# Optimization experiments

Hardware: AMD Instinct MI355X
Metric: run time of the kernel (lower is better)

The kernel has to match this reference:

```python
import jax, jax.numpy as jnp
import numpy as np

B, N, H = 32, 2048, 128
L4H = 4 * H  # concatenated (c0,h0,c1,h1) embedding dim


def _lstm_cell(x, c, h, Wx, Wh, b):
    g = x @ Wx + h @ Wh + b                      # [B,N,4H]
    i, f, gg, o = jnp.split(g, 4, axis=-1)
    c_new = jax.nn.sigmoid(f) * c + jax.nn.sigmoid(i) * jnp.tanh(gg)
    h_new = jax.nn.sigmoid(o) * jnp.tanh(c_new)
    return c_new, h_new


def setup_inputs() -> dict:
    key = jax.random.key(0)
    ks = jax.random.split(key, 20)
    s = 0.05
    inp = {
        'node_embeddings': jax.random.normal(ks[0], (B, N, H), jnp.float32),
        'c0': jax.random.normal(ks[1], (B, N, H), jnp.float32),
        'h0': jax.random.normal(ks[2], (B, N, H), jnp.float32),
        'c1': jax.random.normal(ks[3], (B, N, H), jnp.float32),
        'h1': jax.random.normal(ks[4], (B, N, H), jnp.float32),
        'instruction_pointer': jax.random.uniform(ks[5], (B, N), jnp.float32),
        'Wx0': s * jax.random.normal(ks[6], (H, 4 * H), jnp.float32),
        'Wh0': s * jax.random.normal(ks[7], (H, 4 * H), jnp.float32),
        'b0': jnp.zeros((4 * H,), jnp.float32),
        'Wx1': s * jax.random.normal(ks[8], (H, 4 * H), jnp.float32),
        'Wh1': s * jax.random.normal(ks[9], (H, 4 * H), jnp.float32),
        'b1': jnp.zeros((4 * H,), jnp.float32),
        'raise_W': s * jax.random.normal(ks[10], (L4H, 2), jnp.float32),
        'raise_b': jnp.zeros((2,), jnp.float32),
        'branch_W': s * jax.random.normal(ks[11], (L4H, 2), jnp.float32),
        'branch_b': jnp.zeros((2,), jnp.float32),
        'true_indexes': jax.random.randint(ks[12], (B, N), 0, N, jnp.int32),
        'false_indexes': jax.random.randint(ks[13], (B, N), 0, N, jnp.int32),
        'raise_indexes': jax.random.randint(ks[14], (B, N), 0, N, jnp.int32),
        'exit_node_indexes': jax.random.randint(ks[15], (B,), 0, N, jnp.int32),
        'raise_node_indexes': jax.random.randint(ks[16], (B,), 0, N, jnp.int32),
        'current_step': jnp.zeros((B,), jnp.int32),
        'step_limits': jax.random.randint(ks[17], (B,), 1, 100, jnp.int32),
    }
    return inp


def reference(node_embeddings, c0, h0, c1, h1, instruction_pointer,
              Wx0, Wh0, b0, Wx1, Wh1, b1, raise_W, raise_b, branch_W, branch_b,
              true_indexes, false_indexes, raise_indexes,
              exit_node_indexes, raise_node_indexes, current_step, step_limits):
    num_nodes = node_embeddings.shape[1]

    # --- execute: stacked 2-layer LSTM per node (vectorized over B,N) ---
    c0n, h0n = _lstm_cell(node_embeddings, c0, h0, Wx0, Wh0, b0)
    c1n, h1n = _lstm_cell(h0n, c1, h1, Wx1, Wh1, b1)
    old = (c0, h0, c1, h1)
    contrib = (c0n, h0n, c1n, h1n)

    # --- mask exit and raise nodes: keep old hidden state there ---
    node_ids = jnp.arange(num_nodes)[None, :]                  # [1,N]
    m_exit = node_ids == exit_node_indexes[:, None]            # [B,N]
    m_raise = node_ids == raise_node_indexes[:, None]          # [B,N]
    m_keep = (m_exit | m_raise)[..., None]                     # raise_in_ipagnn=True
    contrib = tuple(jnp.where(m_keep, o, c) for o, c in zip(old, contrib))

    # --- raise / branch decisions ---
    emb = jnp.concatenate(contrib, axis=-1)                    # [B,N,4H]
    raise_dec = jax.nn.softmax(emb @ raise_W + raise_b, axis=-1)
    raise_dec = jnp.where(m_exit[..., None], jnp.array([0.0, 1.0], raise_dec.dtype), raise_dec)
    branch_dec = jax.nn.softmax(emb @ branch_W + branch_b, axis=-1)

    p_raise = raise_dec[..., 0]
    p_noraise = raise_dec[..., 1]
    p_true = p_noraise * branch_dec[..., 0]
    p_false = p_noraise * branch_dec[..., 1]

    seg = jax.vmap(lambda d, i: jax.ops.segment_sum(d, i, num_segments=num_nodes))

    # --- instruction pointer update (scatter-add over soft edges) ---
    ip = instruction_pointer
    ip_new = (seg(p_raise * ip, raise_indexes)
              + seg(p_true * ip, true_indexes)
              + seg(p_false * ip, false_indexes))               # [B,N]

    # --- hidden-state aggregation, weighted by instruction pointer ---
    denom = (ip_new + 1e-7)[..., None]                          # [B,N,1]
    wr = (p_raise * ip)[..., None]
    wt = (p_true * ip)[..., None]
    wf = (p_false * ip)[..., None]
    agg = tuple((seg(hc * wr, raise_indexes)
                 + seg(hc * wt, true_indexes)
                 + seg(hc * wf, false_indexes)) / denom
                for hc in contrib)

    # --- keep old state if example already hit its step limit ---
    live = (current_step < step_limits)                         # [B]
    ip_fin = jnp.where(live[:, None], ip_new, ip)
    hid_fin = tuple(jnp.where(live[:, None, None], a, o) for a, o in zip(agg, old))

    # pack carry: (c0,h0,c1,h1) embedding + instruction pointer -> [B,N,4H+1]
    return jnp.concatenate(list(hid_fin) + [ip_fin[..., None]], axis=-1)
```

## Files before the change

### kernel.cpp

```cpp
#include <hip/hip_runtime.h>
#include <hip/hip_bf16.h>

constexpr int Bc  = 32;
constexpr int Nc  = 2048;
constexpr int Hc  = 128;
constexpr int H4c = 512;
constexpr int BNc = Bc * Nc;

typedef __attribute__((ext_vector_type(8))) short short8;
typedef __attribute__((ext_vector_type(4))) float f32x4;

__device__ __forceinline__ float sigf(float x)  { return 1.f / (1.f + __expf(-x)); }
__device__ __forceinline__ float tanh_(float x) { return 1.f - 2.f / (__expf(2.f * x) + 1.f); }

__device__ __forceinline__ unsigned short bfu(float f) {
    union { float f; unsigned u; } a; a.f = f;
    unsigned u = a.u;
    return (unsigned short)((u + 0x7FFFu + ((u >> 16) & 1u)) >> 16);
}
__device__ __forceinline__ float bf2f(unsigned short u) {
    union { unsigned u; float f; } a; a.u = ((unsigned)u) << 16;
    return a.f;
}
__device__ __forceinline__ unsigned cvtpk(float lo, float hi) {
    unsigned r;
    asm("v_cvt_pk_bf16_f32 %0, %1, %2" : "=v"(r) : "v"(lo), "v"(hi));
    return r;
}

__device__ __forceinline__ int cs_off(int row, int unit) {
    return row * 512 + ((unit ^ (row & 7)) << 4);
}

__global__ __launch_bounds__(256) void prep_kernel(
    const float* __restrict__ Wx0, const float* __restrict__ Wh0,
    const float* __restrict__ Wx1, const float* __restrict__ Wh1,
    unsigned short* __restrict__ W0F, unsigned short* __restrict__ W1F)
{
    int idx = blockIdx.x * 256 + threadIdx.x;
    int ct = idx >> 9, ks = (idx >> 6) & 7, lane = idx & 63;
    int col = ct * 16 + (lane & 15);
    unsigned short* p0 = W0F + (size_t)idx * 8;
    unsigned short* p1 = W1F + (size_t)idx * 8;
    #pragma unroll
    for (int e = 0; e < 8; ++e) {
        int k = ks * 32 + (lane >> 4) * 8 + e;
        float v0 = (k < 128) ? Wx0[k * 512 + col] : Wh0[(k - 128) * 512 + col];
        float v1 = (k < 128) ? Wx1[k * 512 + col] : Wh1[(k - 128) * 512 + col];
        p0[e] = bfu(v0);
        p1[e] = bfu(v1);
    }
}

__global__ __launch_bounds__(512, 4) void gemm0_kernel(
    const float* __restrict__ x_in,  const float* __restrict__ c0_in,
    const float* __restrict__ h0_in, const float* __restrict__ h1_in,
    const unsigned short* __restrict__ W0F, const float* __restrict__ b0,
    const int* __restrict__ exit_i, const int* __restrict__ raise_i,
    unsigned short* __restrict__ contrib, unsigned short* __restrict__ A1F)
{
    __shared__ __align__(16) char AsCs[32768];

    const int t    = threadIdx.x;
    const int w    = t >> 6, l = t & 63, lr = l & 15, lg = l >> 4;
    const int row0 = blockIdx.x * 64;
    const int bidx = row0 >> 11;
    const int eb   = exit_i[bidx];
    const int rbn  = raise_i[bidx];
    const int j    = w * 16 + lr;

    {
        const int r = t >> 3, q = t & 7;
        #pragma unroll
        for (int i = 0; i < 4; ++i) {
            const int u = q + i * 8;
            const float* sp = (u < 16 ? x_in : h0_in)
                + (size_t)(row0 + r) * Hc + (u & 15) * 8;
            float4 v0 = ((const float4*)sp)[0];
            float4 v1 = ((const float4*)sp)[1];
            uint4 wv = { cvtpk(v0.x, v0.y), cvtpk(v0.z, v0.w),
                         cvtpk(v1.x, v1.y), cvtpk(v1.z, v1.w) };
            *(uint4*)(AsCs + cs_off(r, u)) = wv;
        }
    }

    f32x4 acc[4][4];
    #pragma unroll
    for (int g = 0; g < 4; ++g) {
        float bv = b0[g * 128 + j];
        f32x4 vv = {bv, bv, bv, bv};
        #pragma unroll
        for (int mt = 0; mt < 4; ++mt) acc[mt][g] = vv;
    }
    short8 bn[4];
    #pragma unroll
    for (int g = 0; g < 4; ++g)
        bn[g] = *(const short8*)(W0F + ((size_t)((g * 8 + w) * 8) * 64 + l) * 8);

    __syncthreads();

    #pragma unroll
    for (int ks = 0; ks < 8; ++ks) {
        short8 bc[4];
        #pragma unroll
        for (int g = 0; g < 4; ++g) bc[g] = bn[g];
        if (ks < 7) {
            #pragma unroll
            for (int g = 0; g < 4; ++g)
                bn[g] = *(const short8*)(W0F + ((size_t)((g * 8 + w) * 8 + ks + 1) * 64 + l) * 8);
        }
        short8 a[4];
        #pragma unroll
        for (int mt = 0; mt < 4; ++mt)
            a[mt] = *(const short8*)(AsCs + cs_off(mt * 16 + lr, ks * 4 + lg));
        #pragma unroll
        for (int mt = 0; mt < 4; ++mt)
            #pragma unroll
            for (int g = 0; g < 4; ++g)
                acc[mt][g] = __builtin_amdgcn_mfma_f32_16x16x32_bf16(
                    a[mt], bc[g], acc[mt][g], 0, 0, 0);
    }

    float c0v[16], h1v[16];
    #pragma unroll
    for (int e = 0; e < 16; ++e) {
        const int grow = row0 + (e >> 2) * 16 + lg * 4 + (e & 3);
        c0v[e] = c0_in[(size_t)grow * Hc + j];
        h1v[e] = h1_in[(size_t)grow * Hc + j];
    }

    __syncthreads();
    char* Cs = AsCs;

    unsigned hnp[4][4];
    #pragma unroll
    for (int mt = 0; mt < 4; ++mt) {
        #pragma unroll
        for (int rr = 0; rr < 4; ++rr) {
            const int e    = mt * 4 + rr;
            const int row  = mt * 16 + lg * 4 + rr;
            const int grow = row0 + row;
            const int n    = grow & (Nc - 1);
            float cold = c0v[e];
            float ig = sigf(acc[mt][0][rr]);
            float fg = sigf(acc[mt][1][rr]);
            float gv = tanh_(acc[mt][2][rr]);
            float og = sigf(acc[mt][3][rr]);
            float cn = fg * cold + ig * gv;
            float hn = og * tanh_(cn);
            const bool keep = (n == eb) || (n == rbn);
            float cw = keep ? cold : cn;
            float hw = hn;
            if (keep) hw = h0_in[(size_t)grow * Hc + j];
            float cwn = __shfl_xor(cw, 1);
            float hwn = __shfl_xor(hw, 1);
            if (!(lr & 1)) {
                *(unsigned*)(Cs + cs_off(row, j >> 3) + (j & 7) * 2)        = cvtpk(cw, cwn);
                *(unsigned*)(Cs + cs_off(row, 16 + (j >> 3)) + (j & 7) * 2) = cvtpk(hw, hwn);
            }
            hnp[mt][rr] = cvtpk(hn, h1v[e]);
        }
    }
    __syncthreads();
    #pragma unroll
    for (int i = 0; i < 4; ++i) {
        const int idx = i * 512 + t;
        const int r = idx >> 5, u = idx & 31;
        short8 v = *(const short8*)(Cs + cs_off(r, u));
        *(short8*)(contrib + (size_t)(row0 + r) * H4c + u * 8) = v;
    }
    __syncthreads();
    #pragma unroll
    for (int mt = 0; mt < 4; ++mt)
        #pragma unroll
        for (int rr = 0; rr < 4; ++rr) {
            const int row = mt * 16 + lg * 4 + rr;
            unsigned pn = __shfl_xor(hnp[mt][rr], 1);
            if (!(lr & 1)) {
                unsigned h0d = (hnp[mt][rr] & 0xFFFFu) | (pn << 16);
                unsigned h1d = (hnp[mt][rr] >> 16) | (pn & 0xFFFF0000u);
                *(unsigned*)(Cs + cs_off(row, j >> 3) + (j & 7) * 2)        = h0d;
                *(unsigned*)(Cs + cs_off(row, 16 + (j >> 3)) + (j & 7) * 2) = h1d;
            }
        }
    __syncthreads();
    #pragma unroll
    for (int i = 0; i < 4; ++i) {
        const int idx  = i * 512 + t;
        const int frag = idx >> 6;
        const int lane = idx & 63;
        const int mt = frag >> 3, ks = frag & 7;
        const int row  = mt * 16 + (lane & 15);
        const int unit = ks * 4 + (lane >> 4);
        short8 v = *(const short8*)(Cs + cs_off(row, unit));
        *(short8*)(A1F + (((size_t)blockIdx.x * 32 + frag) << 9) + (size_t)lane * 8) = v;
    }
}

__global__ __launch_bounds__(512, 4) void gemm1_kernel(
    const unsigned short* __restrict__ A1F, const float* __restrict__ c1_in,
    const float* __restrict__ h1_in,
    const unsigned short* __restrict__ W1F, const float* __restrict__ b1,
    const float* __restrict__ rW, const float* __restrict__ rbv,
    const float* __restrict__ bW, const float* __restrict__ bbv,
    const float* __restrict__ ip_in,
    const int* __restrict__ exit_i, const int* __restrict__ raise_i,
    unsigned short* __restrict__ contrib, float* __restrict__ w_all)
{
    __shared__ __align__(16) char AsCs[32768];
    __shared__ __align__(16) float dw[2048];

    const int t    = threadIdx.x;
    const int w    = t >> 6, l = t & 63, lr = l & 15, lg = l >> 4;
    const int row0 = blockIdx.x * 64;
    const int bidx = row0 >> 11;
    const int eb   = exit_i[bidx];
    const int rbn  = raise_i[bidx];
    const int j    = w * 16 + lr;

    const unsigned short* Af = A1F + ((size_t)blockIdx.x * 32 << 9);
    #pragma unroll
    for (int c = 0; c < 4; ++c) {
        const int frag = w * 4 + c;
        __builtin_amdgcn_global_load_lds(
            (const unsigned int*)(Af + ((size_t)frag * 64 + l) * 8),
            (unsigned int*)(AsCs + frag * 1024), 16, 0, 0);
    }
    if (t < 256) {
        ((float4*)dw)[t]       = ((const float4*)rW)[t];
        ((float4*)dw)[256 + t] = ((const float4*)bW)[t];
    }

    f32x4 acc[4][4];
    #pragma unroll
    for (int g = 0; g < 4; ++g) {
        float bv = b1[g * 128 + j];
        f32x4 vv = {bv, bv, bv, bv};
        #pragma unroll
        for (int mt = 0; mt < 4; ++mt) acc[mt][g] = vv;
    }
    short8 bn[4];
    #pragma unroll
    for (int g = 0; g < 4; ++g)
        bn[g] = *(const short8*)(W1F + ((size_t)((g * 8 + w) * 8) * 64 + l) * 8);

    __syncthreads();

    #pragma unroll
    for (int ks = 0; ks < 8; ++ks) {
        short8 bc[4];
        #pragma unroll
        for (int g = 0; g < 4; ++g) bc[g] = bn[g];
        if (ks < 7) {
            #pragma unroll
            for (int g = 0; g < 4; ++g)
                bn[g] = *(const short8*)(W1F + ((size_t)((g * 8 + w) * 8 + ks + 1) * 64 + l) * 8);
        }
        short8 a[4];
        #pragma unroll
        for (int mt = 0; mt < 4; ++mt)
            a[mt] = *(const short8*)(AsCs + (mt * 8 + ks) * 1024 + l * 16);
        #pragma unroll
        for (int mt = 0; mt < 4; ++mt)
            #pragma unroll
            for (int g = 0; g < 4; ++g)
                acc[mt][g] = __builtin_amdgcn_mfma_f32_16x16x32_bf16(
                    a[mt], bc[g], acc[mt][g], 0, 0, 0);
    }

    float c1v[16];
    #pragma unroll
    for (int e = 0; e < 16; ++e) {
        const int grow = row0 + (e >> 2) * 16 + lg * 4 + (e & 3);
        c1v[e] = c1_in[(size_t)grow * Hc + j];
    }

    __syncthreads();
    char* Cs = AsCs;

    #pragma unroll
    for (int mt = 0; mt < 4; ++mt) {
        #pragma unroll
        for (int rr = 0; rr < 4; ++rr) {
            const int e    = mt * 4 + rr;
            const int row  = mt * 16 + lg * 4 + rr;
            const int grow = row0 + row;
            const int n    = grow & (Nc - 1);
            float cold = c1v[e];
            float ig = sigf(acc[mt][0][rr]);
            float fg = sigf(acc[mt][1][rr]);
            float gv = tanh_(acc[mt][2][rr]);
            float og = sigf(acc[mt][3][rr]);
            float cn = fg * cold + ig * gv;
            float hn = og * tanh_(cn);
            const bool keep = (n == eb) || (n == rbn);
            float cw = keep ? cold : cn;
            float hw = hn;
            if (keep) hw = h1_in[(size_t)grow * Hc + j];
            float cwn = __shfl_xor(cw, 1);
            float hwn = __shfl_xor(hw, 1);
            if (!(lr & 1)) {
                *(unsigned*)(Cs + cs_off(row, j >> 3) + (j & 7) * 2)        = cvtpk(cw, cwn);
                *(unsigned*)(Cs + cs_off(row, 16 + (j >> 3)) + (j & 7) * 2) = cvtpk(hw, hwn);
            }
        }
    }
    __syncthreads();

    #pragma unroll
    for (int i = 0; i < 4; ++i) {
        const int idx = i * 512 + t;
        const int r = idx >> 5, u = idx & 31;
        short8 v = *(const short8*)(Cs + cs_off(r, u));
        *(short8*)(contrib + (size_t)(row0 + r) * H4c + 256 + u * 8) = v;
    }

    {
        const int r8 = l >> 3, s = l & 7;
        const int row  = w * 8 + r8;
        const int grow = row0 + row;
        float pr0 = 0.f, pr1 = 0.f, pb0 = 0.f, pb1 = 0.f;
        #pragma unroll
        for (int cu = 0; cu < 8; ++cu) {
            short8 ev;
            if (s < 4)
                ev = *(const short8*)(contrib + (size_t)grow * H4c + s * 64 + cu * 8);
            else
                ev = *(const short8*)(Cs + cs_off(row, (s - 4) * 8 + cu));
            const int col0 = s * 64 + cu * 8;
            const float4* rp = (const float4*)(dw + col0 * 2);
            const float4* bp = (const float4*)(dw + 1024 + col0 * 2);
            #pragma unroll
            for (int q = 0; q < 4; ++q) {
                float4 rv = rp[q], bv = bp[q];
                float e0 = bf2f((unsigned short)ev[q * 2]);
                float e1 = bf2f((unsigned short)ev[q * 2 + 1]);
                pr0 += e0 * rv.x + e1 * rv.z;
                pr1 += e0 * rv.y + e1 * rv.w;
                pb0 += e0 * bv.x + e1 * bv.z;
                pb1 += e0 * bv.y + e1 * bv.w;
            }
        }
        #pragma unroll
        for (int m = 1; m < 8; m <<= 1) {
            pr0 += __shfl_xor(pr0, m);
            pr1 += __shfl_xor(pr1, m);
            pb0 += __shfl_xor(pb0, m);
            pb1 += __shfl_xor(pb1, m);
        }
        if (s == 0) {
            const int n = grow & (Nc - 1);
            float r0v = pr0 + rbv[0], r1v = pr1 + rbv[1];
            float m  = fmaxf(r0v, r1v);
            float z0 = __expf(r0v - m), z1 = __expf(r1v - m);
            float inv = 1.f / (z0 + z1);
            float praise = z0 * inv, pno = z1 * inv;
            if (n == eb) { praise = 0.f; pno = 1.f; }
            float q0 = pb0 + bbv[0], q1 = pb1 + bbv[1];
            float mm = fmaxf(q0, q1);
            float y0 = __expf(q0 - mm), y1 = __expf(q1 - mm);
            float binv = 1.f / (y0 + y1);
            float ipv = ip_in[grow];
            w_all[grow]            = praise * ipv;
            w_all[BNc + grow]      = pno * y0 * binv * ipv;
            w_all[2 * BNc + grow]  = pno * y1 * binv * ipv;
        }
    }
}

__global__ __launch_bounds__(256) void build_kernel(
    const int* __restrict__ t_idx, const int* __restrict__ f_idx,
    const int* __restrict__ r_idx, int* __restrict__ head, int* __restrict__ nxt)
{
    const int row  = blockIdx.x * 256 + threadIdx.x;
    const int base = (row >> 11) << 11;
    const int e0 = row * 4;
    int o;
    o = atomicExch(&head[base + r_idx[row]], e0);     nxt[e0]     = o;
    o = atomicExch(&head[base + t_idx[row]], e0 + 1); nxt[e0 + 1] = o;
    o = atomicExch(&head[base + f_idx[row]], e0 + 2); nxt[e0 + 2] = o;
}

__global__ __launch_bounds__(256) void gather_kernel(
    const unsigned short* __restrict__ contrib, const float* __restrict__ w_all,
    const int* __restrict__ head, const int* __restrict__ nxt,
    const float* __restrict__ c0_in, const float* __restrict__ h0_in,
    const float* __restrict__ c1_in, const float* __restrict__ h1_in,
    const float* __restrict__ ip_in,
    const int* __restrict__ cstep, const int* __restrict__ slim,
    float* __restrict__ out)
{
    const int gtid = blockIdx.x * 256 + threadIdx.x;
    const int wid  = gtid >> 6;
    const int l    = gtid & 63;
    const int bidx = wid >> 11;

    float acc[8] = {0.f, 0.f, 0.f, 0.f, 0.f, 0.f, 0.f, 0.f};
    float ipsum = 0.f;

    int e = head[wid];
    while (e >= 0) {
        const int src = e >> 2;
        const float w = w_all[(e & 3) * BNc + src];
        const unsigned short* crow = contrib + (size_t)src * 512;
        #pragma unroll
        for (int q = 0; q < 8; ++q) acc[q] += w * bf2f(crow[q * 64 + l]);
        ipsum += w;
        e = nxt[e];
    }

    const bool live = cstep[bidx] < slim[bidx];
    float* orow = out + (size_t)wid * 513;
    if (live) {
        const float inv = 1.f / (ipsum + 1e-7f);
        #pragma unroll
        for (int q = 0; q < 8; ++q) orow[q * 64 + l] = acc[q] * inv;
        if (l == 0) orow[512] = ipsum;
    } else {
        #pragma unroll
        for (int q = 0; q < 8; ++q) {
            const int off = (q & 1) * 64 + l;
            const float* p = (q >> 1) == 0 ? c0_in : (q >> 1) == 1 ? h0_in
                           : (q >> 1) == 2 ? c1_in : h1_in;
            orow[q * 64 + l] = p[(size_t)wid * Hc + off];
        }
        if (l == 0) orow[512] = ip_in[wid];
    }
}

extern "C" void kernel_launch(void* const* d_in, const int* in_sizes, int n_in,
                              void* d_out, int out_size, void* d_ws, size_t ws_size,
                              hipStream_t stream) {
    const float* x     = (const float*)d_in[0];
    const float* c0    = (const float*)d_in[1];
    const float* h0    = (const float*)d_in[2];
    const float* c1    = (const float*)d_in[3];
    const float* h1    = (const float*)d_in[4];
    const float* ip    = (const float*)d_in[5];
    const float* Wx0   = (const float*)d_in[6];
    const float* Wh0   = (const float*)d_in[7];
    const float* b0    = (const float*)d_in[8];
    const float* Wx1   = (const float*)d_in[9];
    const float* Wh1   = (const float*)d_in[10];
    const float* b1    = (const float*)d_in[11];
    const float* rW    = (const float*)d_in[12];
    const float* rb    = (const float*)d_in[13];
    const float* bW    = (const float*)d_in[14];
    const float* bb    = (const float*)d_in[15];
    const int* t_idx   = (const int*)d_in[16];
    const int* f_idx   = (const int*)d_in[17];
    const int* r_idx   = (const int*)d_in[18];
    const int* exit_i  = (const int*)d_in[19];
    const int* raise_i = (const int*)d_in[20];
    const int* cstep   = (const int*)d_in[21];
    const int* slim    = (const int*)d_in[22];
    float* out = (float*)d_out;

    unsigned short* contrib = (unsigned short*)d_ws;
    unsigned short* A1F = contrib + (size_t)BNc * 512;
    unsigned short* W0F = A1F + (size_t)BNc * 256;
    unsigned short* W1F = W0F + 512 * 256;
    float* w_all = (float*)(W1F + 512 * 256);
    int*   head  = (int*)(w_all + 3 * (size_t)BNc);
    int*   nxt   = head + BNc;

    hipMemsetAsync(head, 0xFF, BNc * sizeof(int), stream);

    prep_kernel<<<64, 256, 0, stream>>>(Wx0, Wh0, Wx1, Wh1, W0F, W1F);
    gemm0_kernel<<<BNc / 64, 512, 0, stream>>>(x, c0, h0, h1, W0F, b0,
                                               exit_i, raise_i, contrib, A1F);
    gemm1_kernel<<<BNc / 64, 512, 0, stream>>>(A1F, c1, h1, W1F, b1,
                                               rW, rb, bW, bb, ip,
                                               exit_i, raise_i, contrib, w_all);
    build_kernel<<<BNc / 256, 256, 0, stream>>>(t_idx, f_idx, r_idx, head, nxt);
    gather_kernel<<<BNc / 4, 256, 0, stream>>>(contrib, w_all, head, nxt,
                                               c0, h0, c1, h1, ip, cstep, slim, out);
}
```

Measured before the change: 219.7 us.

## Drop A1F fragment buffer; gemm1 builds its A tile from contrib and h1

gemm0 no longer writes a pre-fragmented bf16 A1F buffer. gemm1 now loads the h0 slice of contrib and converts h1 from fp32 directly into LDS, which removes a 32 MB write/read round trip and two LDS staging passes in gemm0. It also changes launch_bounds occupancy from 4 to 2 and loads c0/c1 inline in the epilogue instead of prefetching them into registers. The trade-offs are that gemm1 re-reads h1 as fp32, uses plain loads instead of global_load_lds, and the c loads are no longer hoisted ahead of the epilogue.

```diff
diff --git a/kernel.cpp b/kernel.cpp
--- a/kernel.cpp
+++ b/kernel.cpp
@@ -52,12 +52,12 @@
     }
 }
 
-__global__ __launch_bounds__(512, 4) void gemm0_kernel(
+__global__ __launch_bounds__(512, 2) void gemm0_kernel(
     const float* __restrict__ x_in,  const float* __restrict__ c0_in,
-    const float* __restrict__ h0_in, const float* __restrict__ h1_in,
+    const float* __restrict__ h0_in,
     const unsigned short* __restrict__ W0F, const float* __restrict__ b0,
     const int* __restrict__ exit_i, const int* __restrict__ raise_i,
-    unsigned short* __restrict__ contrib, unsigned short* __restrict__ A1F)
+    unsigned short* __restrict__ contrib)
 {
     __shared__ __align__(16) char AsCs[32768];
 
@@ -121,27 +121,17 @@
                     a[mt], bc[g], acc[mt][g], 0, 0, 0);
     }
 
-    float c0v[16], h1v[16];
-    #pragma unroll
-    for (int e = 0; e < 16; ++e) {
-        const int grow = row0 + (e >> 2) * 16 + lg * 4 + (e & 3);
-        c0v[e] = c0_in[(size_t)grow * Hc + j];
-        h1v[e] = h1_in[(size_t)grow * Hc + j];
-    }
-
     __syncthreads();
     char* Cs = AsCs;
 
-    unsigned hnp[4][4];
     #pragma unroll
     for (int mt = 0; mt < 4; ++mt) {
         #pragma unroll
         for (int rr = 0; rr < 4; ++rr) {
-            const int e    = mt * 4 + rr;
             const int row  = mt * 16 + lg * 4 + rr;
             const int grow = row0 + row;
             const int n    = grow & (Nc - 1);
-            float cold = c0v[e];
+            float cold = c0_in[(size_t)grow * Hc + j];
             float ig = sigf(acc[mt][0][rr]);
             float fg = sigf(acc[mt][1][rr]);
             float gv = tanh_(acc[mt][2][rr]);
@@ -158,7 +148,6 @@
                 *(unsigned*)(Cs + cs_off(row, j >> 3) + (j & 7) * 2)        = cvtpk(cw, cwn);
                 *(unsigned*)(Cs + cs_off(row, 16 + (j >> 3)) + (j & 7) * 2) = cvtpk(hw, hwn);
             }
-            hnp[mt][rr] = cvtpk(hn, h1v[e]);
         }
     }
     __syncthreads();
@@ -169,36 +158,10 @@
         short8 v = *(const short8*)(Cs + cs_off(r, u));
         *(short8*)(contrib + (size_t)(row0 + r) * H4c + u * 8) = v;
     }
-    __syncthreads();
-    #pragma unroll
-    for (int mt = 0; mt < 4; ++mt)
-        #pragma unroll
-        for (int rr = 0; rr < 4; ++rr) {
-            const int row = mt * 16 + lg * 4 + rr;
-            unsigned pn = __shfl_xor(hnp[mt][rr], 1);
-            if (!(lr & 1)) {
-                unsigned h0d = (hnp[mt][rr] & 0xFFFFu) | (pn << 16);
-                unsigned h1d = (hnp[mt][rr] >> 16) | (pn & 0xFFFF0000u);
-                *(unsigned*)(Cs + cs_off(row, j >> 3) + (j & 7) * 2)        = h0d;
-                *(unsigned*)(Cs + cs_off(row, 16 + (j >> 3)) + (j & 7) * 2) = h1d;
-            }
-        }
-    __syncthreads();
-    #pragma unroll
-    for (int i = 0; i < 4; ++i) {
-        const int idx  = i * 512 + t;
-        const int frag = idx >> 6;
-        const int lane = idx & 63;
-        const int mt = frag >> 3, ks = frag & 7;
-        const int row  = mt * 16 + (lane & 15);
-        const int unit = ks * 4 + (lane >> 4);
-        short8 v = *(const short8*)(Cs + cs_off(row, unit));
-        *(short8*)(A1F + (((size_t)blockIdx.x * 32 + frag) << 9) + (size_t)lane * 8) = v;
-    }
-}
-
-__global__ __launch_bounds__(512, 4) void gemm1_kernel(
-    const unsigned short* __restrict__ A1F, const float* __restrict__ c1_in,
+}
+
+__global__ __launch_bounds__(512, 2) void gemm1_kernel(
+    const unsigned short* __restrict__ contrib_r, const float* __restrict__ c1_in,
     const float* __restrict__ h1_in,
     const unsigned short* __restrict__ W1F, const float* __restrict__ b1,
     const float* __restrict__ rW, const float* __restrict__ rbv,
@@ -218,13 +181,24 @@
     const int rbn  = raise_i[bidx];
     const int j    = w * 16 + lr;
 
-    const unsigned short* Af = A1F + ((size_t)blockIdx.x * 32 << 9);
-    #pragma unroll
-    for (int c = 0; c < 4; ++c) {
-        const int frag = w * 4 + c;
-        __builtin_amdgcn_global_load_lds(
-            (const unsigned int*)(Af + ((size_t)frag * 64 + l) * 8),
-            (unsigned int*)(AsCs + frag * 1024), 16, 0, 0);
+    {
+        const int r = t >> 3, q = t & 7;
+        #pragma unroll
+        for (int i = 0; i < 2; ++i) {
+            const int u = q * 2 + i;
+            short8 v = *(const short8*)(contrib_r + (size_t)(row0 + r) * H4c + 128 + u * 8);
+            *(short8*)(AsCs + cs_off(r, u)) = v;
+        }
+        #pragma unroll
+        for (int i = 0; i < 2; ++i) {
+            const int u = q * 2 + i;
+            const float* sp = h1_in + (size_t)(row0 + r) * Hc + u * 8;
+            float4 v0 = ((const float4*)sp)[0];
+            float4 v1 = ((const float4*)sp)[1];
+            uint4 wv = { cvtpk(v0.x, v0.y), cvtpk(v0.z, v0.w),
+                         cvtpk(v1.x, v1.y), cvtpk(v1.z, v1.w) };
+            *(uint4*)(AsCs + cs_off(r, 16 + u)) = wv;
+        }
     }
     if (t < 256) {
         ((float4*)dw)[t]       = ((const float4*)rW)[t];
@@ -259,7 +233,7 @@
         short8 a[4];
         #pragma unroll
         for (int mt = 0; mt < 4; ++mt)
-            a[mt] = *(const short8*)(AsCs + (mt * 8 + ks) * 1024 + l * 16);
+            a[mt] = *(const short8*)(AsCs + cs_off(mt * 16 + lr, ks * 4 + lg));
         #pragma unroll
         for (int mt = 0; mt < 4; ++mt)
             #pragma unroll
@@ -268,13 +242,6 @@
                     a[mt], bc[g], acc[mt][g], 0, 0, 0);
     }
 
-    float c1v[16];
-    #pragma unroll
-    for (int e = 0; e < 16; ++e) {
-        const int grow = row0 + (e >> 2) * 16 + lg * 4 + (e & 3);
-        c1v[e] = c1_in[(size_t)grow * Hc + j];
-    }
-
     __syncthreads();
     char* Cs = AsCs;
 
@@ -282,11 +249,10 @@
     for (int mt = 0; mt < 4; ++mt) {
         #pragma unroll
         for (int rr = 0; rr < 4; ++rr) {
-            const int e    = mt * 4 + rr;
             const int row  = mt * 16 + lg * 4 + rr;
             const int grow = row0 + row;
             const int n    = grow & (Nc - 1);
-            float cold = c1v[e];
+            float cold = c1_in[(size_t)grow * Hc + j];
             float ig = sigf(acc[mt][0][rr]);
             float fg = sigf(acc[mt][1][rr]);
             float gv = tanh_(acc[mt][2][rr]);
@@ -324,7 +290,7 @@
         for (int cu = 0; cu < 8; ++cu) {
             short8 ev;
             if (s < 4)
-                ev = *(const short8*)(contrib + (size_t)grow * H4c + s * 64 + cu * 8);
+                ev = *(const short8*)(contrib_r + (size_t)grow * H4c + s * 64 + cu * 8);
             else
                 ev = *(const short8*)(Cs + cs_off(row, (s - 4) * 8 + cu));
             const int col0 = s * 64 + cu * 8;
@@ -457,8 +423,7 @@
     float* out = (float*)d_out;
 
     unsigned short* contrib = (unsigned short*)d_ws;
-    unsigned short* A1F = contrib + (size_t)BNc * 512;
-    unsigned short* W0F = A1F + (size_t)BNc * 256;
+    unsigned short* W0F = contrib + (size_t)BNc * 512;
     unsigned short* W1F = W0F + 512 * 256;
     float* w_all = (float*)(W1F + 512 * 256);
     int*   head  = (int*)(w_all + 3 * (size_t)BNc);
@@ -467,9 +432,9 @@
     hipMemsetAsync(head, 0xFF, BNc * sizeof(int), stream);
 
     prep_kernel<<<64, 256, 0, stream>>>(Wx0, Wh0, Wx1, Wh1, W0F, W1F);
-    gemm0_kernel<<<BNc / 64, 512, 0, stream>>>(x, c0, h0, h1, W0F, b0,
-                                               exit_i, raise_i, contrib, A1F);
-    gemm1_kernel<<<BNc / 64, 512, 0, stream>>>(A1F, c1, h1, W1F, b1,
+    gemm0_kernel<<<BNc / 64, 512, 0, stream>>>(x, c0, h0, W0F, b0,
+                                               exit_i, raise_i, contrib);
+    gemm1_kernel<<<BNc / 64, 512, 0, stream>>>(contrib, c1, h1, W1F, b1,
                                                rW, rb, bW, bb, ip,
                                                exit_i, raise_i, contrib, w_all);
     build_kernel<<<BNc / 256, 256, 0, stream>>>(t_idx, f_idx, r_idx, head, nxt);
```

New measurement: 247.6 us. +12.7%, slower.
